# Performance work log

Measured on AMD Instinct MI355X. Metric: run time of the kernel, lower is better.

## Reference

```python
import jax, jax.numpy as jnp
import numpy as np

LOG2PI = float(np.log(2.0 * np.pi))

INPUT_DIM, HIDDEN_DIM, OUTPUT_DIM, HORIZON = 128, 2048, 128, 1024


def setup_inputs() -> dict:
    key = jax.random.key(0)
    ks = jax.random.split(key, 10)
    s = 0.02
    return {
        "s0": jax.random.normal(ks[0], (HORIZON, INPUT_DIM), jnp.float32),
        "eps": jax.random.normal(ks[1], (HORIZON, OUTPUT_DIM), jnp.float32),
        "W_ih": jax.random.normal(ks[2], (4 * HIDDEN_DIM, INPUT_DIM), jnp.float32) * s,
        "W_hh": jax.random.normal(ks[3], (4 * HIDDEN_DIM, HIDDEN_DIM), jnp.float32) * s,
        "b_ih": jax.random.normal(ks[4], (4 * HIDDEN_DIM,), jnp.float32) * s,
        "b_hh": jax.random.normal(ks[5], (4 * HIDDEN_DIM,), jnp.float32) * s,
        "W_mu": jax.random.normal(ks[6], (OUTPUT_DIM, HIDDEN_DIM), jnp.float32) * s,
        "b_mu": jax.random.normal(ks[7], (OUTPUT_DIM,), jnp.float32) * s,
        "W_lv": jax.random.normal(ks[8], (OUTPUT_DIM, HIDDEN_DIM), jnp.float32) * s,
        "b_lv": jax.random.normal(ks[9], (OUTPUT_DIM,), jnp.float32) * s,
        "H": HORIZON,
    }


def reference(s0, eps, W_ih, W_hh, b_ih, b_hh, W_mu, b_mu, W_lv, b_lv, H):
    hd = W_hh.shape[1]

    def step(carry, inp):
        h, c = carry  # [hidden], [hidden]
        x, e = inp    # [input_dim], [output_dim]
        gates = W_ih @ x + b_ih + W_hh @ h + b_hh  # [4*hidden]
        i, f, g, o = jnp.split(gates, 4)
        i, f, o = jax.nn.sigmoid(i), jax.nn.sigmoid(f), jax.nn.sigmoid(o)
        g = jnp.tanh(g)
        c = f * c + i * g
        h = o * jnp.tanh(c)
        mu = W_mu @ h + b_mu
        logvar = W_lv @ h + b_lv
        std = jnp.exp(0.5 * logvar)
        # Normal.sample() is detached from the graph in torch
        x_samp = jax.lax.stop_gradient(mu + std * e)
        lp = -0.5 * jnp.square((x_samp - mu) / std) - jnp.log(std) - 0.5 * LOG2PI
        return (h, c), (x_samp, lp, h)

    h0 = jnp.zeros((hd,), s0.dtype)
    c0 = jnp.zeros((hd,), s0.dtype)
    _, (xs, lps, hs) = jax.lax.scan(step, (h0, c0), (s0[:H], eps[:H]))
    return xs, lps, hs  # [H, out], [H, out], [H, hidden]
```

## Files before the change

kernel.cpp:

```cpp
#include <hip/hip_runtime.h>
#include <math.h>

#define TSTEPS 1024
#define HID    2048
#define IN_D   128
#define OUT_D  128
#define NWG    256
#define NTHR   512
#define NPAIRS (HID / 2)

#define LOG2PI_F 1.8378770664093453f

typedef unsigned long long u64;
typedef unsigned int       u32;

static __device__ __forceinline__ u32 bf16_rne(float f) {
    u32 u = __float_as_uint(f);
    return (u + 0x7FFFu + ((u >> 16) & 1u)) >> 16;
}
static __device__ __forceinline__ float bf16_lo(u32 payload) {
    return __uint_as_float(payload << 16);
}
static __device__ __forceinline__ float bf16_hi(u32 payload) {
    return __uint_as_float(payload & 0xFFFF0000u);
}
static __device__ __forceinline__ float fast_sig(float x) {
    return __builtin_amdgcn_rcpf(1.0f + __expf(-x));
}
static __device__ __forceinline__ float fast_tanh(float x) {
    return 1.0f - 2.0f * __builtin_amdgcn_rcpf(1.0f + __expf(2.0f * x));
}

__global__ __launch_bounds__(NTHR)
void lstm_persist(const float* __restrict__ s0,
                  const float* __restrict__ Wih,
                  const float* __restrict__ Whh,
                  const float* __restrict__ bih,
                  const float* __restrict__ bhh,
                  float* __restrict__ hs_out,
                  u64* __restrict__ pairs)
{
    __shared__ __align__(16) float4 ldsH[2][HID / 4];
    __shared__ __align__(16) u64    cellbuf[8];

    const int tid   = threadIdx.x;
    const int wg    = blockIdx.x;
    const int hbase = wg * 8;
    const int rg    = tid >> 6;
    const int lane  = tid & 63;
    const int cell  = hbase + rg;

    float w[4][32];
    float wih2[4][2];
    float breg[4];
#pragma unroll
    for (int m = 0; m < 4; ++m) {
        const int grow = m * HID + cell;
        const float4* src = (const float4*)(Whh + (size_t)grow * HID + lane * 32);
#pragma unroll
        for (int q = 0; q < 8; ++q) {
            float4 v = src[q];
            w[m][4*q+0] = v.x; w[m][4*q+1] = v.y;
            w[m][4*q+2] = v.z; w[m][4*q+3] = v.w;
        }
        wih2[m][0] = Wih[(size_t)grow * IN_D + 2 * lane];
        wih2[m][1] = Wih[(size_t)grow * IN_D + 2 * lane + 1];
        breg[m]    = bih[grow] + bhh[grow];
    }

    float c = 0.0f;

    for (int t = 0; t < TSTEPS; ++t) {
        const int slot = (t - 1) & 1;

        const float2 xv = *(const float2*)(s0 + (size_t)t * IN_D + 2 * lane);
        float acc[4];
#pragma unroll
        for (int m = 0; m < 4; ++m)
            acc[m] = wih2[m][0] * xv.x + wih2[m][1] * xv.y;

        if (t > 0) {
            const u32 want = (u32)t;
            const u64* sp = pairs + (size_t)slot * NPAIRS + rg * 128 + 2 * lane;
            u64 q0, q1;
            for (;;) {
                q0 = __hip_atomic_load(sp,     __ATOMIC_RELAXED, __HIP_MEMORY_SCOPE_AGENT);
                q1 = __hip_atomic_load(sp + 1, __ATOMIC_RELAXED, __HIP_MEMORY_SCOPE_AGENT);
                const int ok = ((u32)(q0 >> 32) == want) & ((u32)(q1 >> 32) == want);
                if (__all(ok)) break;
                __builtin_amdgcn_s_sleep(1);
            }
            float4 hv;
            hv.x = bf16_lo((u32)q0);
            hv.y = bf16_hi((u32)q0);
            hv.z = bf16_lo((u32)q1);
            hv.w = bf16_hi((u32)q1);
            const int cch = rg * 64 + lane;
            ldsH[slot][cch ^ ((cch >> 3) & 7)] = hv;
        }
        __syncthreads();

        if (t > 0) {
#pragma unroll
            for (int j = 0; j < 8; ++j) {
                const int p = (8 * lane + j) ^ (lane & 7);
                float4 hv = ldsH[slot][p];
#pragma unroll
                for (int m = 0; m < 4; ++m) {
                    acc[m] += hv.x * w[m][4*j+0];
                    acc[m] += hv.y * w[m][4*j+1];
                    acc[m] += hv.z * w[m][4*j+2];
                    acc[m] += hv.w * w[m][4*j+3];
                }
            }
        }

#pragma unroll
        for (int m = 0; m < 4; ++m) {
            acc[m] += __shfl_xor(acc[m], 1);
            acc[m] += __shfl_xor(acc[m], 2);
            acc[m] += __shfl_xor(acc[m], 4);
            acc[m] += __shfl_xor(acc[m], 8);
            acc[m] += __shfl_xor(acc[m], 16);
            acc[m] += __shfl_xor(acc[m], 32);
        }

        if (lane == 0) {
            const float ig = fast_sig (acc[0] + breg[0]);
            const float fg = fast_sig (acc[1] + breg[1]);
            const float gg = fast_tanh(acc[2] + breg[2]);
            const float og = fast_sig (acc[3] + breg[3]);
            c = fg * c + ig * gg;
            const float h = og * fast_tanh(c);
            cellbuf[rg] = ((u64)bf16_rne(h) << 32) | (u64)__float_as_uint(h);
        }
        __syncthreads();

        if (tid < 4) {
            const u64 cb0 = cellbuf[2 * tid];
            const u64 cb1 = cellbuf[2 * tid + 1];
            const u64 pair = (((u64)(u32)(t + 1)) << 32)
                           | (u64)(((u32)(cb0 >> 32)) | (((u32)(cb1 >> 32)) << 16));
            __hip_atomic_store(&pairs[(size_t)(t & 1) * NPAIRS + wg * 4 + tid], pair,
                               __ATOMIC_RELAXED, __HIP_MEMORY_SCOPE_AGENT);
            *(float2*)&hs_out[(size_t)t * HID + hbase + 2 * tid] =
                make_float2(__uint_as_float((u32)cb0), __uint_as_float((u32)cb1));
        }
    }
}

__global__ __launch_bounds__(256)
void out_head(const float* __restrict__ eps,
              const float* __restrict__ Wmu,
              const float* __restrict__ bmu,
              const float* __restrict__ Wlv,
              const float* __restrict__ blv,
              const float* __restrict__ hs,
              float* __restrict__ xs,
              float* __restrict__ lp)
{
    __shared__ __align__(16) float hlds[4][HID];
    __shared__ __align__(16) float exch[4][256];

    const int tid = threadIdx.x;
    const int t0  = blockIdx.x * 4;

    {
        const float4* src = (const float4*)(hs + (size_t)t0 * HID);
        float4* dst = (float4*)&hlds[0][0];
#pragma unroll
        for (int i = 0; i < 8; ++i)
            dst[tid + i * 256] = src[tid + i * 256];
    }
    __syncthreads();

    const int  jrow  = tid & 127;
    const bool is_lv = tid >= 128;
    const float* Wrow = (is_lv ? Wlv : Wmu) + (size_t)jrow * HID;
    const float  bias = is_lv ? blv[jrow] : bmu[jrow];

    float acc[4] = {0.f, 0.f, 0.f, 0.f};
    const float4* w4 = (const float4*)Wrow;
#pragma unroll 4
    for (int kq = 0; kq < HID / 4; ++kq) {
        float4 wv = w4[kq];
#pragma unroll
        for (int tt = 0; tt < 4; ++tt) {
            float4 hv = ((const float4*)&hlds[tt][0])[kq];
            acc[tt] += wv.x * hv.x + wv.y * hv.y + wv.z * hv.z + wv.w * hv.w;
        }
    }
#pragma unroll
    for (int tt = 0; tt < 4; ++tt) exch[tt][tid] = acc[tt] + bias;
    __syncthreads();

#pragma unroll
    for (int r = 0; r < 2; ++r) {
        const int item = tid + r * 256;
        const int tt = item >> 7;
        const int jj = item & 127;
        const int t  = t0 + tt;
        const float mu = exch[tt][jj];
        const float lv = exch[tt][128 + jj];
        const float e  = eps[(size_t)t * OUT_D + jj];
        const float sd = expf(0.5f * lv);
        const float x  = mu + sd * e;
        const float d  = (x - mu) / sd;
        const float l  = -0.5f * d * d - 0.5f * lv - 0.5f * LOG2PI_F;
        xs[(size_t)t * OUT_D + jj] = x;
        lp[(size_t)t * OUT_D + jj] = l;
    }
}

extern "C" void kernel_launch(void* const* d_in, const int* in_sizes, int n_in,
                              void* d_out, int out_size, void* d_ws, size_t ws_size,
                              hipStream_t stream)
{
    (void)in_sizes; (void)n_in; (void)out_size; (void)ws_size;

    const float* s0  = (const float*)d_in[0];
    const float* eps = (const float*)d_in[1];
    const float* Wih = (const float*)d_in[2];
    const float* Whh = (const float*)d_in[3];
    const float* bih = (const float*)d_in[4];
    const float* bhh = (const float*)d_in[5];
    const float* Wmu = (const float*)d_in[6];
    const float* bmu = (const float*)d_in[7];
    const float* Wlv = (const float*)d_in[8];
    const float* blv = (const float*)d_in[9];

    float* out = (float*)d_out;
    float* xs = out;
    float* lp = out + TSTEPS * OUT_D;
    float* hs = out + 2 * TSTEPS * OUT_D;

    u64* pairs = (u64*)d_ws;

    (void)hipMemsetAsync(d_ws, 0, 2 * NPAIRS * sizeof(u64), stream);

    hipLaunchKernelGGL(lstm_persist, dim3(NWG), dim3(NTHR), 0, stream,
                       s0, Wih, Whh, bih, bhh, hs, pairs);

    hipLaunchKernelGGL(out_head, dim3(TSTEPS / 4), dim3(256), 0, stream,
                       eps, Wmu, bmu, Wlv, blv, hs, xs, lp);
}
```

Measured before the change: 2.947 ms.

## Repartition LSTM recurrent matvec across wave halves and drop LDS h broadcast

```diff
diff --git a/kernel.cpp b/kernel.cpp
--- a/kernel.cpp
+++ b/kernel.cpp
@@ -31,7 +31,7 @@
     return 1.0f - 2.0f * __builtin_amdgcn_rcpf(1.0f + __expf(2.0f * x));
 }
 
-__global__ __launch_bounds__(NTHR)
+__global__ __launch_bounds__(NTHR, 2)
 void lstm_persist(const float* __restrict__ s0,
                   const float* __restrict__ Wih,
                   const float* __restrict__ Whh,
@@ -40,111 +40,147 @@
                   float* __restrict__ hs_out,
                   u64* __restrict__ pairs)
 {
-    __shared__ __align__(16) float4 ldsH[2][HID / 4];
-    __shared__ __align__(16) u64    cellbuf[8];
+    __shared__ __align__(16) float gpart[2][8][32];
 
     const int tid   = threadIdx.x;
     const int wg    = blockIdx.x;
     const int hbase = wg * 8;
     const int rg    = tid >> 6;
     const int lane  = tid & 63;
-    const int cell  = hbase + rg;
-
-    float w[4][32];
-    float wih2[4][2];
-    float breg[4];
-#pragma unroll
-    for (int m = 0; m < 4; ++m) {
-        const int grow = m * HID + cell;
-        const float4* src = (const float4*)(Whh + (size_t)grow * HID + lane * 32);
-#pragma unroll
-        for (int q = 0; q < 8; ++q) {
-            float4 v = src[q];
-            w[m][4*q+0] = v.x; w[m][4*q+1] = v.y;
-            w[m][4*q+2] = v.z; w[m][4*q+3] = v.w;
-        }
-        wih2[m][0] = Wih[(size_t)grow * IN_D + 2 * lane];
-        wih2[m][1] = Wih[(size_t)grow * IN_D + 2 * lane + 1];
-        breg[m]    = bih[grow] + bhh[grow];
+    const int H     = lane >> 5;
+    const int sl    = lane & 31;
+
+    float w[16][8];
+    const int k0 = 256 * rg + 8 * sl;
+#pragma unroll
+    for (int r = 0; r < 16; ++r) {
+        const int li   = 16 * H + r;
+        const int grow = (li >> 3) * HID + hbase + (li & 7);
+        const float4* src = (const float4*)(Whh + (size_t)grow * HID + k0);
+        float4 a = src[0], b = src[1];
+        w[r][0] = a.x; w[r][1] = a.y; w[r][2] = a.z; w[r][3] = a.w;
+        w[r][4] = b.x; w[r][5] = b.y; w[r][6] = b.z; w[r][7] = b.w;
+    }
+    float wihr[16];
+    const int xk = 16 * rg + sl;
+#pragma unroll
+    for (int r = 0; r < 16; ++r) wihr[r] = 0.f;
+    if (sl < 16) {
+#pragma unroll
+        for (int r = 0; r < 16; ++r) {
+            const int li   = 16 * H + r;
+            const int grow = (li >> 3) * HID + hbase + (li & 7);
+            wihr[r] = Wih[(size_t)grow * IN_D + xk];
+        }
+    }
+    float breg = 0.f;
+    if (rg == 0 && lane < 32) {
+        const int grow = (lane >> 3) * HID + hbase + (lane & 7);
+        breg = bih[grow] + bhh[grow];
     }
 
     float c = 0.0f;
 
     for (int t = 0; t < TSTEPS; ++t) {
-        const int slot = (t - 1) & 1;
-
-        const float2 xv = *(const float2*)(s0 + (size_t)t * IN_D + 2 * lane);
-        float acc[4];
-#pragma unroll
-        for (int m = 0; m < 4; ++m)
-            acc[m] = wih2[m][0] * xv.x + wih2[m][1] * xv.y;
+        const float xv = (sl < 16) ? s0[(size_t)t * IN_D + xk] : 0.f;
+        float acc[16];
+#pragma unroll
+        for (int r = 0; r < 16; ++r) acc[r] = wihr[r] * xv;
 
         if (t > 0) {
             const u32 want = (u32)t;
-            const u64* sp = pairs + (size_t)slot * NPAIRS + rg * 128 + 2 * lane;
-            u64 q0, q1;
+            const u64* sp = pairs + (size_t)((t - 1) & 1) * NPAIRS + 128 * rg + 4 * sl;
+            u64 q0, q1, q2, q3;
             for (;;) {
-                q0 = __hip_atomic_load(sp,     __ATOMIC_RELAXED, __HIP_MEMORY_SCOPE_AGENT);
+                q0 = __hip_atomic_load(sp + 0, __ATOMIC_RELAXED, __HIP_MEMORY_SCOPE_AGENT);
                 q1 = __hip_atomic_load(sp + 1, __ATOMIC_RELAXED, __HIP_MEMORY_SCOPE_AGENT);
-                const int ok = ((u32)(q0 >> 32) == want) & ((u32)(q1 >> 32) == want);
+                q2 = __hip_atomic_load(sp + 2, __ATOMIC_RELAXED, __HIP_MEMORY_SCOPE_AGENT);
+                q3 = __hip_atomic_load(sp + 3, __ATOMIC_RELAXED, __HIP_MEMORY_SCOPE_AGENT);
+                const int ok = ((u32)(q0 >> 32) == want) & ((u32)(q1 >> 32) == want)
+                             & ((u32)(q2 >> 32) == want) & ((u32)(q3 >> 32) == want);
                 if (__all(ok)) break;
                 __builtin_amdgcn_s_sleep(1);
             }
-            float4 hv;
-            hv.x = bf16_lo((u32)q0);
-            hv.y = bf16_hi((u32)q0);
-            hv.z = bf16_lo((u32)q1);
-            hv.w = bf16_hi((u32)q1);
-            const int cch = rg * 64 + lane;
-            ldsH[slot][cch ^ ((cch >> 3) & 7)] = hv;
+            const float h0 = bf16_lo((u32)q0), h1 = bf16_hi((u32)q0);
+            const float h2 = bf16_lo((u32)q1), h3 = bf16_hi((u32)q1);
+            const float h4 = bf16_lo((u32)q2), h5 = bf16_hi((u32)q2);
+            const float h6 = bf16_lo((u32)q3), h7 = bf16_hi((u32)q3);
+#pragma unroll
+            for (int r = 0; r < 16; ++r) {
+                acc[r] += h0 * w[r][0] + h1 * w[r][1] + h2 * w[r][2] + h3 * w[r][3]
+                        + h4 * w[r][4] + h5 * w[r][5] + h6 * w[r][6] + h7 * w[r][7];
+            }
+        }
+
+        {
+            const bool u1 = lane & 1;
+#pragma unroll
+            for (int i = 0; i < 8; ++i) {
+                const float send = u1 ? acc[i] : acc[i + 8];
+                const float recv = __shfl_xor(send, 1);
+                acc[i] = (u1 ? acc[i + 8] : acc[i]) + recv;
+            }
+            const bool u2 = lane & 2;
+#pragma unroll
+            for (int i = 0; i < 4; ++i) {
+                const float send = u2 ? acc[i] : acc[i + 4];
+                const float recv = __shfl_xor(send, 2);
+                acc[i] = (u2 ? acc[i + 4] : acc[i]) + recv;
+            }
+            const bool u4 = lane & 4;
+#pragma unroll
+            for (int i = 0; i < 2; ++i) {
+                const float send = u4 ? acc[i] : acc[i + 2];
+                const float recv = __shfl_xor(send, 4);
+                acc[i] = (u4 ? acc[i + 2] : acc[i]) + recv;
+            }
+            const bool u8 = lane & 8;
+            {
+                const float send = u8 ? acc[0] : acc[1];
+                const float recv = __shfl_xor(send, 8);
+                acc[0] = (u8 ? acc[1] : acc[0]) + recv;
+            }
+            acc[0] += __shfl_xor(acc[0], 16);
+        }
+
+        const int par = t & 1;
+        if ((lane & 16) == 0) {
+            const int sb    = lane & 15;
+            const int rstar = ((sb & 1) << 3) | ((sb & 2) << 1)
+                            | ((sb & 4) >> 1) | ((sb & 8) >> 3);
+            gpart[par][rg][16 * H + rstar] = acc[0];
         }
         __syncthreads();
 
-        if (t > 0) {
-#pragma unroll
-            for (int j = 0; j < 8; ++j) {
-                const int p = (8 * lane + j) ^ (lane & 7);
-                float4 hv = ldsH[slot][p];
-#pragma unroll
-                for (int m = 0; m < 4; ++m) {
-                    acc[m] += hv.x * w[m][4*j+0];
-                    acc[m] += hv.y * w[m][4*j+1];
-                    acc[m] += hv.z * w[m][4*j+2];
-                    acc[m] += hv.w * w[m][4*j+3];
-                }
-            }
-        }
-
-#pragma unroll
-        for (int m = 0; m < 4; ++m) {
-            acc[m] += __shfl_xor(acc[m], 1);
-            acc[m] += __shfl_xor(acc[m], 2);
-            acc[m] += __shfl_xor(acc[m], 4);
-            acc[m] += __shfl_xor(acc[m], 8);
-            acc[m] += __shfl_xor(acc[m], 16);
-            acc[m] += __shfl_xor(acc[m], 32);
-        }
-
-        if (lane == 0) {
-            const float ig = fast_sig (acc[0] + breg[0]);
-            const float fg = fast_sig (acc[1] + breg[1]);
-            const float gg = fast_tanh(acc[2] + breg[2]);
-            const float og = fast_sig (acc[3] + breg[3]);
-            c = fg * c + ig * gg;
-            const float h = og * fast_tanh(c);
-            cellbuf[rg] = ((u64)bf16_rne(h) << 32) | (u64)__float_as_uint(h);
-        }
-        __syncthreads();
-
-        if (tid < 4) {
-            const u64 cb0 = cellbuf[2 * tid];
-            const u64 cb1 = cellbuf[2 * tid + 1];
-            const u64 pair = (((u64)(u32)(t + 1)) << 32)
-                           | (u64)(((u32)(cb0 >> 32)) | (((u32)(cb1 >> 32)) << 16));
-            __hip_atomic_store(&pairs[(size_t)(t & 1) * NPAIRS + wg * 4 + tid], pair,
-                               __ATOMIC_RELAXED, __HIP_MEMORY_SCOPE_AGENT);
-            *(float2*)&hs_out[(size_t)t * HID + hbase + 2 * tid] =
-                make_float2(__uint_as_float((u32)cb0), __uint_as_float((u32)cb1));
+        if (rg == 0) {
+            float g = 0.f;
+            if (lane < 32) {
+                g = breg;
+#pragma unroll
+                for (int k = 0; k < 8; ++k) g += gpart[par][k][lane];
+            }
+            const int j = lane & 7;
+            const float zi = __shfl(g, j);
+            const float zf = __shfl(g, j + 8);
+            const float zg = __shfl(g, j + 16);
+            const float zo = __shfl(g, j + 24);
+            float h = 0.f;
+            if (lane < 8) {
+                const float ig = fast_sig(zi);
+                const float fg = fast_sig(zf);
+                const float gg = fast_tanh(zg);
+                const float og = fast_sig(zo);
+                c = fg * c + ig * gg;
+                h = og * fast_tanh(c);
+                hs_out[(size_t)t * HID + hbase + lane] = h;
+            }
+            const float ho = __shfl_xor(h, 1);
+            if (lane < 8 && (lane & 1) == 0) {
+                const u64 pair = (((u64)(u32)(t + 1)) << 32)
+                               | (u64)(bf16_rne(h) | (bf16_rne(ho) << 16));
+                __hip_atomic_store(&pairs[(size_t)(t & 1) * NPAIRS + wg * 4 + (lane >> 1)],
+                                   pair, __ATOMIC_RELAXED, __HIP_MEMORY_SCOPE_AGENT);
+            }
         }
     }
 }
```

Measured after the change: 3.716 ms. +26.1%, slower.
